# Kernel optimization log

Measured on AMD Instinct MI355X. Metric: run time of the kernel, lower is better.

The kernel has to match this reference:

```python
import jax, jax.numpy as jnp
import numpy as np

N_NODES = 100000
N_EDGES = 800000
N_IN = 256
N_H = 128


def setup_inputs() -> dict:
    key = jax.random.key(0)
    ks = jax.random.split(key, 8)
    x_1 = jax.random.normal(ks[0], (1, N_NODES, N_IN), dtype=jnp.float32)
    x_2 = jax.random.normal(ks[1], (1, N_NODES, N_IN), dtype=jnp.float32)
    edge_index = jax.random.randint(ks[2], (2, N_EDGES), 0, N_NODES, dtype=jnp.int32)
    edge_weight = jax.random.uniform(ks[3], (N_EDGES,), dtype=jnp.float32)
    # xavier-uniform-ish init for fc weight (stored as [in, out])
    lim = float(np.sqrt(6.0 / (N_IN + N_H)))
    W_gcn = jax.random.uniform(ks[4], (N_IN, N_H), minval=-lim, maxval=lim, dtype=jnp.float32)
    gcn_bias = jnp.zeros((N_H,), dtype=jnp.float32)
    prelu_a = jnp.full((1,), 0.25, dtype=jnp.float32)  # PReLU default slope
    lim2 = float(np.sqrt(1.0 / N_H))
    lin_W = jax.random.uniform(ks[5], (N_H, N_H), minval=-lim2, maxval=lim2, dtype=jnp.float32)
    lin_b = jax.random.uniform(ks[6], (N_H,), minval=-lim2, maxval=lim2, dtype=jnp.float32)
    return {
        "x_1": x_1, "x_2": x_2, "edge_index": edge_index, "edge_weight": edge_weight,
        "W_gcn": W_gcn, "gcn_bias": gcn_bias, "prelu_a": prelu_a,
        "lin_W": lin_W, "lin_b": lin_b,
    }


def _prelu(x, a):
    return jnp.where(x >= 0, x, a * x)


def _gcn(feat, edge_index, edge_weight, W, b, a, n_nodes):
    # feat: [1, N, n_in] -> h: [N, n_h]
    h = jnp.squeeze(feat, 0) @ W
    row, col = edge_index[0], edge_index[1]
    # spmm: out[i] = sum_{e: row_e = i} w_e * h[col_e]
    msg = edge_weight[:, None] * h[col]            # [E, n_h]
    agg = jax.ops.segment_sum(msg, row, num_segments=n_nodes)  # [N, n_h]
    return _prelu(agg + b, a)                      # [N, n_h]


def reference(x_1, x_2, edge_index, edge_weight, W_gcn, gcn_bias, prelu_a, lin_W, lin_b):
    n = x_1.shape[1]
    h_1 = _gcn(x_1, edge_index, edge_weight, W_gcn, gcn_bias, prelu_a, n)
    h_2 = _gcn(x_2, edge_index, edge_weight, W_gcn, gcn_bias, prelu_a, n)
    z_1 = (h_1 @ lin_W + lin_b).sum(1)   # [N]
    z_2 = (h_2 @ lin_W + lin_b).sum(1)   # [N]
    return jnp.concatenate((z_1, z_2), 0)  # [2N]
```

## Files before the change

### kernel.cpp

```cpp
#include <hip/hip_runtime.h>

#define N_NODES 100000
#define N_EDGES 800000
#define N_IN    256
#define N_H     128
#define M_TOT   (2 * N_NODES)
#define HB_ROW  256

typedef __bf16 bfx8 __attribute__((ext_vector_type(8)));
typedef unsigned short u16x8 __attribute__((ext_vector_type(8)));
typedef float fx4 __attribute__((ext_vector_type(4)));

__device__ inline unsigned short f2bf(float f) {
    union { float f; unsigned u; } v; v.f = f;
    return (unsigned short)((v.u + 0x7FFF + ((v.u >> 16) & 1)) >> 16);
}
__device__ inline float bf2f(unsigned short s) {
    union { unsigned u; float f; } v; v.u = ((unsigned)s) << 16;
    return v.f;
}

#define WT_S 264
#define NGB  1563

__global__ __launch_bounds__(512, 4) void gemm_kernel(
        const float* __restrict__ x1, const float* __restrict__ x2,
        const unsigned short* __restrict__ wT,
        unsigned short* __restrict__ hb) {
    __shared__ unsigned short wl[N_H * WT_S];
    const int t = threadIdx.x;
#pragma unroll
    for (int i = 0; i < 8; ++i) {
        int f  = t + i * 512;
        int n  = f >> 5;
        int kp = (f & 31) * 8;
        *(u16x8*)(wl + n * WT_S + kp) = *(const u16x8*)(wT + n * N_IN + kp);
    }
    __syncthreads();

    const int wave = t >> 6, lane = t & 63;
    const int quad = lane >> 4, l16 = lane & 15;
    const int mw = blockIdx.x * 128 + wave * 16;
    if (mw >= M_TOT) return;
    const int half = (mw < N_NODES) ? 0 : 1;
    const float* x = half ? x2 : x1;
    const int mrow = half ? mw - N_NODES : mw;

    fx4 acc[8];
#pragma unroll
    for (int c = 0; c < 8; ++c) acc[c] = (fx4){0.f, 0.f, 0.f, 0.f};

    const float* xrow = x + (size_t)(mrow + l16) * N_IN;
#pragma unroll
    for (int kk = 0; kk < N_IN; kk += 32) {
        float4 a0 = *(const float4*)(xrow + kk + quad * 8);
        float4 a1 = *(const float4*)(xrow + kk + quad * 8 + 4);
        u16x8 au;
        au[0] = f2bf(a0.x); au[1] = f2bf(a0.y); au[2] = f2bf(a0.z); au[3] = f2bf(a0.w);
        au[4] = f2bf(a1.x); au[5] = f2bf(a1.y); au[6] = f2bf(a1.z); au[7] = f2bf(a1.w);
        bfx8 af = __builtin_bit_cast(bfx8, au);
#pragma unroll
        for (int c = 0; c < 8; ++c) {
            bfx8 bf = *(const bfx8*)(wl + (size_t)(c * 16 + l16) * WT_S + kk + quad * 8);
            acc[c] = __builtin_amdgcn_mfma_f32_16x16x32_bf16(af, bf, acc[c], 0, 0, 0);
        }
    }
#pragma unroll
    for (int c = 0; c < 8; ++c)
#pragma unroll
        for (int r = 0; r < 4; ++r)
            hb[(size_t)(mrow + quad * 4 + r) * HB_ROW + half * N_H + c * 16 + l16] =
                f2bf(acc[c][r]);
}

#define HIST_BLKS 3125
__global__ __launch_bounds__(256) void prep_kernel(const int* __restrict__ ei,
                                                   int* __restrict__ deg,
                                                   const float* __restrict__ W,
                                                   unsigned short* __restrict__ wT,
                                                   const float* __restrict__ linW,
                                                   const float* __restrict__ linb,
                                                   float* __restrict__ wsum) {
    const int t = threadIdx.x;
    if (blockIdx.x < HIST_BLKS) {
        int e = blockIdx.x * 256 + t;
        if (e < N_EDGES) atomicAdd(deg + ei[e], 1);
    } else if (blockIdx.x < HIST_BLKS + 32) {
        int kb = (blockIdx.x - HIST_BLKS) * 8;
#pragma unroll
        for (int p = 0; p < 4; ++p) {
            int idx = p * 256 + t;
            int k = kb + (idx >> 7), n = idx & 127;
            wT[(size_t)n * N_IN + k] = f2bf(W[(size_t)k * N_H + n]);
        }
    } else {
        int j = t;
        if (j < N_H) {
            float s = 0.f;
            for (int o = 0; o < N_H; ++o) s += linW[j * N_H + o];
            wsum[j] = s;
        }
        if (j == N_H) {
            float s = 0.f;
            for (int o = 0; o < N_H; ++o) s += linb[o];
            wsum[N_H] = s;
        }
    }
}

__global__ __launch_bounds__(256) void scan1_kernel(const int* __restrict__ deg,
                                                    int* __restrict__ part,
                                                    int* __restrict__ bsum) {
    __shared__ int s[256];
    int g = blockIdx.x * 256 + threadIdx.x;
    int v = (g < N_NODES) ? deg[g] : 0;
    s[threadIdx.x] = v;
    __syncthreads();
#pragma unroll
    for (int off = 1; off < 256; off <<= 1) {
        int t = (threadIdx.x >= off) ? s[threadIdx.x - off] : 0;
        __syncthreads();
        s[threadIdx.x] += t;
        __syncthreads();
    }
    if (g < N_NODES) part[g] = s[threadIdx.x] - v;
    if (threadIdx.x == 255) bsum[blockIdx.x] = s[255];
}

#define NBLK_SCAN 391
__global__ __launch_bounds__(256) void scan3_kernel(const int* __restrict__ part,
                                                    const int* __restrict__ bsum,
                                                    int* __restrict__ off,
                                                    int* __restrict__ cursor) {
    __shared__ int red[256];
    const int t = threadIdx.x;
    int acc = 0;
    for (int j = t; j < (int)blockIdx.x; j += 256) acc += bsum[j];
    red[t] = acc;
    __syncthreads();
#pragma unroll
    for (int o = 128; o; o >>= 1) {
        if (t < o) red[t] += red[t + o];
        __syncthreads();
    }
    const int prefix = red[0];
    int g = blockIdx.x * 256 + t;
    if (g < N_NODES) {
        int o = part[g] + prefix;
        off[g] = o;
        cursor[g] = o;
    }
    if (g == 0) off[N_NODES] = N_EDGES;
}

__global__ __launch_bounds__(256) void scatter_kernel(const int* __restrict__ ei,
                                                      const float* __restrict__ ew,
                                                      int* __restrict__ cursor,
                                                      int2* __restrict__ edata) {
    int e = blockIdx.x * 256 + threadIdx.x;
    if (e >= N_EDGES) return;
    int row = ei[e];
    int pos = atomicAdd(cursor + row, 1);
    edata[pos] = make_int2(ei[N_EDGES + e] * HB_ROW, __float_as_int(ew[e]));
}

__global__ __launch_bounds__(256) void gcn_seg_kernel(const int* __restrict__ off,
                                                      const int2* __restrict__ edata,
                                                      const unsigned short* __restrict__ hb,
                                                      const float* __restrict__ gcn_bias,
                                                      const float* __restrict__ prelu_a,
                                                      const float* __restrict__ wsum,
                                                      float* __restrict__ zout) {
    const int wave = threadIdx.x >> 6, lane = threadIdx.x & 63;
    const int node = blockIdx.x * 4 + wave;
    const int half = lane >> 5;
    const int fl   = (lane & 31) * 4;
    const int o8   = half * N_H + fl;
    const int s = __builtin_amdgcn_readfirstlane(off[node]);
    const int e = __builtin_amdgcn_readfirstlane(off[node + 1]);
    float p0 = 0.f, p1 = 0.f, p2 = 0.f, p3 = 0.f;
    float q0 = 0.f, q1 = 0.f, q2 = 0.f, q3 = 0.f;
    int i = s;
    for (; i + 4 <= e; i += 4) {
        int2 E0 = edata[i], E1 = edata[i + 1], E2 = edata[i + 2], E3 = edata[i + 3];
        ushort4 h0 = *(const ushort4*)(hb + E0.x + o8);
        ushort4 h1 = *(const ushort4*)(hb + E1.x + o8);
        ushort4 h2 = *(const ushort4*)(hb + E2.x + o8);
        ushort4 h3 = *(const ushort4*)(hb + E3.x + o8);
        float w0 = __int_as_float(E0.y), w1 = __int_as_float(E1.y);
        float w2 = __int_as_float(E2.y), w3 = __int_as_float(E3.y);
        p0 += w0 * bf2f(h0.x) + w1 * bf2f(h1.x);
        p1 += w0 * bf2f(h0.y) + w1 * bf2f(h1.y);
        p2 += w0 * bf2f(h0.z) + w1 * bf2f(h1.z);
        p3 += w0 * bf2f(h0.w) + w1 * bf2f(h1.w);
        q0 += w2 * bf2f(h2.x) + w3 * bf2f(h3.x);
        q1 += w2 * bf2f(h2.y) + w3 * bf2f(h3.y);
        q2 += w2 * bf2f(h2.z) + w3 * bf2f(h3.z);
        q3 += w2 * bf2f(h2.w) + w3 * bf2f(h3.w);
    }
    for (; i < e; ++i) {
        int2 E0 = edata[i];
        float w0 = __int_as_float(E0.y);
        ushort4 h0 = *(const ushort4*)(hb + E0.x + o8);
        p0 += w0 * bf2f(h0.x);
        p1 += w0 * bf2f(h0.y);
        p2 += w0 * bf2f(h0.z);
        p3 += w0 * bf2f(h0.w);
    }
    p0 += q0; p1 += q1; p2 += q2; p3 += q3;

    const float alpha = prelu_a[0];
    float4 gb4 = *(const float4*)(gcn_bias + fl);
    float4 ws4 = *(const float4*)(wsum + fl);
    float v0 = p0 + gb4.x, v1 = p1 + gb4.y, v2 = p2 + gb4.z, v3 = p3 + gb4.w;
    v0 = (v0 >= 0.f) ? v0 : alpha * v0;
    v1 = (v1 >= 0.f) ? v1 : alpha * v1;
    v2 = (v2 >= 0.f) ? v2 : alpha * v2;
    v3 = (v3 >= 0.f) ? v3 : alpha * v3;
    float sres = v0 * ws4.x + v1 * ws4.y + v2 * ws4.z + v3 * ws4.w;
#pragma unroll
    for (int o = 16; o; o >>= 1) sres += __shfl_down(sres, o, 32);
    if ((lane & 31) == 0)
        zout[node + half * N_NODES] = sres + wsum[128];
}

extern "C" void kernel_launch(void* const* d_in, const int* in_sizes, int n_in,
                              void* d_out, int out_size, void* d_ws, size_t ws_size,
                              hipStream_t stream) {
    const float* x1 = (const float*)d_in[0];
    const float* x2 = (const float*)d_in[1];
    const int*   ei = (const int*)d_in[2];
    const float* ew = (const float*)d_in[3];
    const float* Wg = (const float*)d_in[4];
    const float* gb = (const float*)d_in[5];
    const float* pa = (const float*)d_in[6];
    const float* lW = (const float*)d_in[7];
    const float* lb = (const float*)d_in[8];
    float* zout = (float*)d_out;

    unsigned short* hb   = (unsigned short*)d_ws;
    int2*  edata  = (int2*)(hb + (size_t)N_NODES * HB_ROW);
    unsigned short* wT   = (unsigned short*)(edata + N_EDGES);
    int*   deg    = (int*)(wT + N_IN * N_H);
    int*   part   = deg + 100096;
    int*   off    = part + 100096;
    int*   cursor = off + 100096;
    int*   bsum   = cursor + 100096;
    float* wsum   = (float*)(bsum + 512);

    hipMemsetAsync(deg, 0, (size_t)N_NODES * sizeof(int), stream);
    prep_kernel<<<HIST_BLKS + 33, 256, 0, stream>>>(ei, deg, Wg, wT, lW, lb, wsum);
    scan1_kernel<<<NBLK_SCAN, 256, 0, stream>>>(deg, part, bsum);
    scan3_kernel<<<NBLK_SCAN, 256, 0, stream>>>(part, bsum, off, cursor);
    scatter_kernel<<<(N_EDGES + 255) / 256, 256, 0, stream>>>(ei, ew, cursor, edata);
    gemm_kernel<<<NGB, 512, 0, stream>>>(x1, x2, wT, hb);
    gcn_seg_kernel<<<N_NODES / 4, 256, 0, stream>>>(off, edata, hb, gb, pa, wsum, zout);
}
```

Before: 399.6 us.

## Pad CSR segments to multiples of four, swizzle GEMM LDS, prefetch X

Each node's edge segment is rounded up to a multiple of four, and the padded slots are zero-filled by a new memset of the edge buffer. This lets the aggregation kernel drop its scalar tail loop and always run the four-wide loop. The GEMM drops the padded LDS stride in favour of an XOR swizzle on the weight tile to avoid bank conflicts. It also double-buffers the global X loads one k-step ahead to hide their latency. The extra memset clears about 9.6 MB each call, and the padding makes edges read in the gather larger.

```diff
diff --git a/kernel.cpp b/kernel.cpp
--- a/kernel.cpp
+++ b/kernel.cpp
@@ -6,6 +6,7 @@
 #define N_H     128
 #define M_TOT   (2 * N_NODES)
 #define HB_ROW  256
+#define E_PAD   1200000
 
 typedef __bf16 bfx8 __attribute__((ext_vector_type(8)));
 typedef unsigned short u16x8 __attribute__((ext_vector_type(8)));
@@ -20,21 +21,21 @@
     return v.f;
 }
 
-#define WT_S 264
-#define NGB  1563
+#define NGB 1563
 
 __global__ __launch_bounds__(512, 4) void gemm_kernel(
         const float* __restrict__ x1, const float* __restrict__ x2,
         const unsigned short* __restrict__ wT,
         unsigned short* __restrict__ hb) {
-    __shared__ unsigned short wl[N_H * WT_S];
+    __shared__ unsigned short wl[N_H * 256];
     const int t = threadIdx.x;
 #pragma unroll
     for (int i = 0; i < 8; ++i) {
         int f  = t + i * 512;
         int n  = f >> 5;
-        int kp = (f & 31) * 8;
-        *(u16x8*)(wl + n * WT_S + kp) = *(const u16x8*)(wT + n * N_IN + kp);
+        int kb = f & 31;
+        *(u16x8*)(wl + n * 256 + ((kb ^ (n & 31)) << 3)) =
+            *(const u16x8*)(wT + n * N_IN + (kb << 3));
     }
     __syncthreads();
 
@@ -50,18 +51,30 @@
 #pragma unroll
     for (int c = 0; c < 8; ++c) acc[c] = (fx4){0.f, 0.f, 0.f, 0.f};
 
-    const float* xrow = x + (size_t)(mrow + l16) * N_IN;
-#pragma unroll
-    for (int kk = 0; kk < N_IN; kk += 32) {
-        float4 a0 = *(const float4*)(xrow + kk + quad * 8);
-        float4 a1 = *(const float4*)(xrow + kk + quad * 8 + 4);
+    const float* xrow = x + (size_t)(mrow + l16) * N_IN + quad * 8;
+
+    float4 pa0 = *(const float4*)(xrow);
+    float4 pb0 = *(const float4*)(xrow + 4);
+    float4 pa1 = *(const float4*)(xrow + 32);
+    float4 pb1 = *(const float4*)(xrow + 36);
+#pragma unroll
+    for (int j = 0; j < 8; ++j) {
+        float4 a0 = (j & 1) ? pa1 : pa0;
+        float4 a1 = (j & 1) ? pb1 : pb0;
+        if (j < 6) {
+            const float4* nx = (const float4*)(xrow + (j + 2) * 32);
+            if (j & 1) { pa1 = nx[0]; pb1 = nx[1]; }
+            else       { pa0 = nx[0]; pb0 = nx[1]; }
+        }
         u16x8 au;
         au[0] = f2bf(a0.x); au[1] = f2bf(a0.y); au[2] = f2bf(a0.z); au[3] = f2bf(a0.w);
         au[4] = f2bf(a1.x); au[5] = f2bf(a1.y); au[6] = f2bf(a1.z); au[7] = f2bf(a1.w);
         bfx8 af = __builtin_bit_cast(bfx8, au);
+        const int kb0 = (j << 2) + quad;
 #pragma unroll
         for (int c = 0; c < 8; ++c) {
-            bfx8 bf = *(const bfx8*)(wl + (size_t)(c * 16 + l16) * WT_S + kk + quad * 8);
+            int n = c * 16 + l16;
+            bfx8 bf = *(const bfx8*)(wl + n * 256 + ((kb0 ^ (n & 31)) << 3));
             acc[c] = __builtin_amdgcn_mfma_f32_16x16x32_bf16(af, bf, acc[c], 0, 0, 0);
         }
     }
@@ -113,7 +126,7 @@
                                                     int* __restrict__ bsum) {
     __shared__ int s[256];
     int g = blockIdx.x * 256 + threadIdx.x;
-    int v = (g < N_NODES) ? deg[g] : 0;
+    int v = (g < N_NODES) ? ((deg[g] + 3) & ~3) : 0;
     s[threadIdx.x] = v;
     __syncthreads();
 #pragma unroll
@@ -130,6 +143,7 @@
 #define NBLK_SCAN 391
 __global__ __launch_bounds__(256) void scan3_kernel(const int* __restrict__ part,
                                                     const int* __restrict__ bsum,
+                                                    const int* __restrict__ deg,
                                                     int* __restrict__ off,
                                                     int* __restrict__ cursor) {
     __shared__ int red[256];
@@ -149,8 +163,8 @@
         int o = part[g] + prefix;
         off[g] = o;
         cursor[g] = o;
-    }
-    if (g == 0) off[N_NODES] = N_EDGES;
+        if (g == N_NODES - 1) off[N_NODES] = o + ((deg[g] + 3) & ~3);
+    }
 }
 
 __global__ __launch_bounds__(256) void scatter_kernel(const int* __restrict__ ei,
@@ -180,8 +194,7 @@
     const int e = __builtin_amdgcn_readfirstlane(off[node + 1]);
     float p0 = 0.f, p1 = 0.f, p2 = 0.f, p3 = 0.f;
     float q0 = 0.f, q1 = 0.f, q2 = 0.f, q3 = 0.f;
-    int i = s;
-    for (; i + 4 <= e; i += 4) {
+    for (int i = s; i < e; i += 4) {
         int2 E0 = edata[i], E1 = edata[i + 1], E2 = edata[i + 2], E3 = edata[i + 3];
         ushort4 h0 = *(const ushort4*)(hb + E0.x + o8);
         ushort4 h1 = *(const ushort4*)(hb + E1.x + o8);
@@ -198,15 +211,6 @@
         q2 += w2 * bf2f(h2.z) + w3 * bf2f(h3.z);
         q3 += w2 * bf2f(h2.w) + w3 * bf2f(h3.w);
     }
-    for (; i < e; ++i) {
-        int2 E0 = edata[i];
-        float w0 = __int_as_float(E0.y);
-        ushort4 h0 = *(const ushort4*)(hb + E0.x + o8);
-        p0 += w0 * bf2f(h0.x);
-        p1 += w0 * bf2f(h0.y);
-        p2 += w0 * bf2f(h0.z);
-        p3 += w0 * bf2f(h0.w);
-    }
     p0 += q0; p1 += q1; p2 += q2; p3 += q3;
 
     const float alpha = prelu_a[0];
@@ -240,7 +244,7 @@
 
     unsigned short* hb   = (unsigned short*)d_ws;
     int2*  edata  = (int2*)(hb + (size_t)N_NODES * HB_ROW);
-    unsigned short* wT   = (unsigned short*)(edata + N_EDGES);
+    unsigned short* wT   = (unsigned short*)(edata + E_PAD);
     int*   deg    = (int*)(wT + N_IN * N_H);
     int*   part   = deg + 100096;
     int*   off    = part + 100096;
@@ -249,9 +253,10 @@
     float* wsum   = (float*)(bsum + 512);
 
     hipMemsetAsync(deg, 0, (size_t)N_NODES * sizeof(int), stream);
+    hipMemsetAsync(edata, 0, (size_t)E_PAD * sizeof(int2), stream);
     prep_kernel<<<HIST_BLKS + 33, 256, 0, stream>>>(ei, deg, Wg, wT, lW, lb, wsum);
     scan1_kernel<<<NBLK_SCAN, 256, 0, stream>>>(deg, part, bsum);
-    scan3_kernel<<<NBLK_SCAN, 256, 0, stream>>>(part, bsum, off, cursor);
+    scan3_kernel<<<NBLK_SCAN, 256, 0, stream>>>(part, bsum, deg, off, cursor);
     scatter_kernel<<<(N_EDGES + 255) / 256, 256, 0, stream>>>(ei, ew, cursor, edata);
     gemm_kernel<<<NGB, 512, 0, stream>>>(x1, x2, wT, hb);
     gcn_seg_kernel<<<N_NODES / 4, 256, 0, stream>>>(off, edata, hb, gb, pa, wsum, zout);
```

Result: no change. 399.2 us (-0.1%).
